# Kernel tuning notes

Hardware: AMD Instinct MI355X
Metric: run time of the kernel (lower is better)

Reference implementation:

```python
import jax, jax.numpy as jnp
from jax import lax
import numpy as np

IMG_W = 384; IMG_H = 384; FEAT = 24; RF = 16
RATIOS = (0.5, 1.0, 2.0); SCALES = (8.0, 16.0, 32.0)
K = 9                      # len(RATIOS) * len(SCALES)
N = FEAT * FEAT * K        # 5184 anchors/proposals
MID = 24; CIN = 512
NMS_THRESH = 0.7; MIN_SIZE = 16.0


def _make_anchors():
    # Faithful port of RPN._get_anchors (vectorized over the grid).
    area = float(RF * RF)
    base = []
    for r in RATIOS:
        cols = np.round(np.sqrt(area / r)); rows = np.round(cols * r)
        x0 = 0.5 * RF - 0.5 * (cols - 1); x1 = 0.5 * RF + 0.5 * (cols - 1)
        y0 = 0.5 * RF - 0.5 * (rows - 1); y1 = 0.5 * RF + 0.5 * (rows - 1)
        aw = x1 - x0 + 1; ah = y1 - y0 + 1
        acx = x0 + 0.5 * (aw - 1); acy = y0 + 0.5 * (ah - 1)
        for s in SCALES:
            nx0 = acx - 0.5 * (aw * s - 1.0); nx1 = acx + 0.5 * (aw * s - 1.0)
            ny0 = acy - 0.5 * (ah * s - 1.0); ny1 = acy + 0.5 * (ah * s - 1.0)
            w = nx1 - nx0 + 1; h = ny1 - ny0 + 1
            base.append([nx0 + 0.5 * (w - 1), ny0 + 0.5 * (h - 1), w, h])
    base = np.asarray(base, np.float32)  # (K,4) as (cx, cy, w, h)
    ii, jj = np.meshgrid(np.arange(FEAT), np.arange(FEAT), indexing='ij')
    g = np.broadcast_to(base, (FEAT, FEAT, K, 4)).copy()  # (H, W, K, 4)
    g[..., 0] += (jj * RF)[:, :, None]
    g[..., 1] += (ii * RF)[:, :, None]
    a = g.reshape(-1, 4)  # matches permute(1,2,0).reshape(-1,4) ordering
    ax0 = a[:, 0] - 0.5 * (a[:, 2] - 1.0); ay0 = a[:, 1] - 0.5 * (a[:, 3] - 1.0)
    ax1 = a[:, 2] + ax0 - 1.0; ay1 = a[:, 3] + ay0 - 1.0
    valid = (ax0 >= 0) & (ay0 >= 0) & (ax1 < IMG_W) & (ay1 < IMG_H)
    return jnp.asarray(a, jnp.float32), jnp.asarray(valid)


def setup_inputs() -> dict:
    key = jax.random.key(0)
    ks = jax.random.split(key, 6)
    anchors, valid_mask = _make_anchors()
    return {
        'x': jax.random.normal(ks[0], (1, CIN, FEAT, FEAT), jnp.float32),
        'labels_class': jax.random.randint(ks[1], (N,), 0, 21, jnp.int32),
        'W_rpn': jax.random.normal(ks[2], (MID, CIN, 3, 3), jnp.float32) * 0.02,
        'b_rpn': jnp.zeros((MID,), jnp.float32),
        'W_cls': jax.random.normal(ks[3], (2 * K, MID), jnp.float32) * 0.05,
        'b_cls': jnp.zeros((2 * K,), jnp.float32),
        'W_reg': jax.random.normal(ks[4], (4 * K, MID), jnp.float32) * 0.01,
        'b_reg': jnp.zeros((4 * K,), jnp.float32),
        'anchors': anchors,
        'valid_mask': valid_mask,
    }


def _forward(x, W_rpn, b_rpn, W_cls, b_cls, W_reg, b_reg, anchors, valid_mask, labels_class):
    # 3x3 conv + relu, then 1x1 cls/reg heads
    h = jax.nn.relu(
        lax.conv_general_dilated(x, W_rpn, (1, 1), ((1, 1), (1, 1)),
                                 dimension_numbers=('NCHW', 'OIHW', 'NCHW'))
        + b_rpn[None, :, None, None])
    cls_out = (jnp.einsum('nchw,oc->nohw', h, W_cls) + b_cls[None, :, None, None])[0]
    cls_out = cls_out.transpose(1, 2, 0).reshape(-1, 2)   # [N,2]
    reg_out = (jnp.einsum('nchw,oc->nohw', h, W_reg) + b_reg[None, :, None, None])[0]
    reg_out = reg_out.transpose(1, 2, 0).reshape(-1, 4)   # [N,4]

    # anchors -> proposals (cx, cy, w, h); computed for all anchors, validity masked below
    ax, ay, aw, ah = anchors[:, 0], anchors[:, 1], anchors[:, 2], anchors[:, 3]
    tx, ty, tw, th = reg_out[:, 0], reg_out[:, 1], reg_out[:, 2], reg_out[:, 3]
    px = ax + aw * tx; py = ay + ah * ty
    pw = aw * jnp.exp(tw); ph = ah * jnp.exp(th)
    proposals = jnp.stack((px, py, pw, ph), axis=1)

    # offset2bbox + clip_boxes
    x0 = px - 0.5 * (pw - 1.0); y0 = py - 0.5 * (ph - 1.0)
    x1 = pw + x0 - 1.0; y1 = ph + y0 - 1.0
    x0 = jnp.clip(x0, 0.0, IMG_W - 1.0); x1 = jnp.clip(x1, 0.0, IMG_W - 1.0)
    y0 = jnp.clip(y0, 0.0, IMG_H - 1.0); y1 = jnp.clip(y1, 0.0, IMG_H - 1.0)
    ws = x1 - x0 + 1.0; hs = y1 - y0 + 1.0

    probs = jax.nn.softmax(cls_out, axis=1)[:, 1]
    validity = valid_mask & (ws >= MIN_SIZE) & (hs >= MIN_SIZE)

    # greedy NMS (padded/masked: invalid boxes get score -1 and are never kept)
    scores = jnp.where(validity, probs, -1.0)
    order = jnp.argsort(-scores)
    bx0, by0, bx1, by1 = x0[order], y0[order], x1[order], y1[order]
    v_sorted = validity[order]
    areas = ws[order] * hs[order]
    iw = jnp.clip(jnp.minimum(bx1[:, None], bx1[None, :]) - jnp.maximum(bx0[:, None], bx0[None, :]) + 1.0, 0.0)
    ih = jnp.clip(jnp.minimum(by1[:, None], by1[None, :]) - jnp.maximum(by0[:, None], by0[None, :]) + 1.0, 0.0)
    inter = iw * ih
    iou = inter / (areas[:, None] + areas[None, :] - inter)  # [N,N]
    idxs = jnp.arange(N)

    def body(sup, xs):
        i, row, v = xs
        keep_i = v & jnp.logical_not(sup[i])
        sup = jnp.where(keep_i, sup | ((row > NMS_THRESH) & (idxs > i)), sup)
        return sup, keep_i

    _, keep_sorted = lax.scan(body, jnp.zeros((N,), bool), (idxs, iou, v_sorted))
    keep = jnp.zeros((N,), bool).at[order].set(keep_sorted)
    keepf = keep.astype(probs.dtype)

    # bbox2offset of kept boxes (padded: suppressed rows zeroed)
    filtered = jnp.stack((x0 + 0.5 * (ws - 1.0), y0 + 0.5 * (hs - 1.0), ws, hs), axis=1) * keepf[:, None]
    probs_kept = probs * keepf
    labels_kept = jnp.where(keep, labels_class, 0)
    return proposals, cls_out, filtered, probs_kept, labels_kept, keep


def reference(x, labels_class, W_rpn, b_rpn, W_cls, b_cls, W_reg, b_reg, anchors, valid_mask):
    return _forward(x, W_rpn, b_rpn, W_cls, b_cls, W_reg, b_reg, anchors, valid_mask, labels_class)
```

## Files before the change

kernel.cpp:

```cpp
#include <hip/hip_runtime.h>
#include <hip/hip_bf16.h>
#include <math.h>

#define NANC   5184
#define NPOS   576
#define CIN    512
#define MIDC   24
#define KANC   9
#define IMGW   384.0f
#define IMGM1  383.0f
#define MINSZ  16.0f
#define THRESH 0.7f

#define OFF_PROP 0
#define OFF_CLS  20736
#define OFF_FILT 31104
#define OFF_PK   51840
#define OFF_LBL  57024
#define OFF_KEEP 62208

#define MCAP 896
#define GCAP 14
#define TOTW (64 * (GCAP*(GCAP+1)/2))

#define WS_XT    0
#define WS_WT    1179648
#define WS_BOX   1622016
#define WS_PROB  1953792
#define WS_KEYS  2036736
#define WS_SIDX  2044928
#define WS_SBOX  2049024
#define WS_MASK  2063360
#define WS_CNT   2117120

__global__ __launch_bounds__(256) void k_prep(const float* __restrict__ x,
                                              const float* __restrict__ W,
                                              float* __restrict__ xt,
                                              float* __restrict__ Wt,
                                              unsigned* cnt) {
    int tid = blockIdx.x * 256 + threadIdx.x;
    if (tid == 0) *cnt = 0;
    const int TOT = CIN * NPOS + MIDC * CIN * 9;
    for (int idx = tid; idx < TOT; idx += gridDim.x * 256) {
        if (idx < CIN * NPOS) {
            int pos = idx >> 9, ic = idx & 511;
            xt[idx] = x[ic * NPOS + pos];
        } else {
            int k = idx - CIN * NPOS;
            int ic = k & 511; int t = k >> 9;
            int oc = t / 9, kk = t % 9;
            Wt[k] = W[(oc * CIN + ic) * 9 + kk];
        }
    }
}

__global__ __launch_bounds__(256) void k_main(
        const float* __restrict__ xt, const float* __restrict__ Wt,
        const float* __restrict__ brpn,
        const float* __restrict__ Wc, const float* __restrict__ bc,
        const float* __restrict__ Wr, const float* __restrict__ br,
        const float* __restrict__ anchors,
        float* __restrict__ out, float4* __restrict__ boxes,
        float* __restrict__ probs, unsigned long long* __restrict__ vkeys,
        unsigned* __restrict__ cnt) {
    const int tid = threadIdx.x;
    const int y = blockIdx.x / 6;
    const int xb = (blockIdx.x % 6) * 4;

    float acc[24][4];
    #pragma unroll
    for (int oc = 0; oc < 24; ++oc)
        #pragma unroll
        for (int p = 0; p < 4; ++p) acc[oc][p] = 0.f;

    for (int half = 0; half < 2; ++half) {
        const int ic = tid + half * 256;
        float xw[3][6];
        #pragma unroll
        for (int r = 0; r < 3; ++r) {
            int yy = y - 1 + r;
            #pragma unroll
            for (int c = 0; c < 6; ++c) {
                int xx = xb - 1 + c;
                bool in = (yy >= 0) & (yy < 24) & (xx >= 0) & (xx < 24);
                xw[r][c] = in ? xt[(yy * 24 + xx) * CIN + ic] : 0.f;
            }
        }
        const float* wp = Wt + ic;
        #pragma unroll
        for (int oc = 0; oc < 24; ++oc) {
            #pragma unroll
            for (int kk = 0; kk < 9; ++kk) {
                const int r = kk / 3, c = kk % 3;
                float wv = wp[(oc * 9 + kk) * CIN];
                #pragma unroll
                for (int p = 0; p < 4; ++p)
                    acc[oc][p] += wv * xw[r][c + p];
            }
        }
    }
    #pragma unroll
    for (int oc = 0; oc < 24; ++oc)
        #pragma unroll
        for (int p = 0; p < 4; ++p) {
            float v = acc[oc][p];
            #pragma unroll
            for (int m = 1; m < 64; m <<= 1) v += __shfl_xor(v, m, 64);
            acc[oc][p] = v;
        }

    __shared__ float red[4][96];
    __shared__ float h_ld[4 * 24];
    __shared__ float cls_ld[4 * 18];
    __shared__ float reg_ld[4 * 36];
    const int wave = tid >> 6, lane = tid & 63;
    if (lane == 0) {
        #pragma unroll
        for (int oc = 0; oc < 24; ++oc)
            #pragma unroll
            for (int p = 0; p < 4; ++p) red[wave][oc * 4 + p] = acc[oc][p];
    }
    __syncthreads();
    if (tid < 96) {
        float s = red[0][tid] + red[1][tid] + red[2][tid] + red[3][tid];
        int oc = tid >> 2, p = tid & 3;
        h_ld[p * 24 + oc] = fmaxf(s + brpn[oc], 0.f);
    }
    __syncthreads();
    if (tid < 216) {
        int p = tid / 54, o = tid % 54;
        const float* hv = h_ld + p * 24;
        if (o < 18) {
            float s = bc[o];
            const float* w = Wc + o * 24;
            #pragma unroll
            for (int c = 0; c < 24; ++c) s += w[c] * hv[c];
            cls_ld[p * 18 + o] = s;
            out[OFF_CLS + (y * 24 + xb + p) * 18 + o] = s;
        } else {
            int o2 = o - 18;
            float s = br[o2];
            const float* w = Wr + o2 * 24;
            #pragma unroll
            for (int c = 0; c < 24; ++c) s += w[c] * hv[c];
            reg_ld[p * 36 + o2] = s;
        }
    }
    __syncthreads();
    if (tid < 36) {
        #pragma clang fp contract(off)
        int p = tid / 9, k = tid % 9;
        int n = (y * 24 + xb + p) * 9 + k;
        float ax = anchors[4 * n], ay = anchors[4 * n + 1];
        float aw = anchors[4 * n + 2], ah = anchors[4 * n + 3];
        float tx = reg_ld[p * 36 + 4 * k],     ty = reg_ld[p * 36 + 4 * k + 1];
        float tw = reg_ld[p * 36 + 4 * k + 2], th = reg_ld[p * 36 + 4 * k + 3];
        float px = ax + aw * tx, py = ay + ah * ty;
        float pw = aw * expf(tw), ph = ah * expf(th);
        out[OFF_PROP + 4 * n]     = px;
        out[OFF_PROP + 4 * n + 1] = py;
        out[OFF_PROP + 4 * n + 2] = pw;
        out[OFF_PROP + 4 * n + 3] = ph;
        float gx0 = ax - 0.5f * (aw - 1.f);
        float gy0 = ay - 0.5f * (ah - 1.f);
        float gx1 = aw + gx0 - 1.f;
        float gy1 = ah + gy0 - 1.f;
        bool geo_ok = (gx0 >= 0.f) & (gy0 >= 0.f) & (gx1 < IMGW) & (gy1 < IMGW);
        float x0 = px - 0.5f * (pw - 1.f);
        float y0 = py - 0.5f * (ph - 1.f);
        float x1 = pw + x0 - 1.f;
        float y1 = ph + y0 - 1.f;
        x0 = fminf(fmaxf(x0, 0.f), IMGM1);
        x1 = fminf(fmaxf(x1, 0.f), IMGM1);
        y0 = fminf(fmaxf(y0, 0.f), IMGM1);
        y1 = fminf(fmaxf(y1, 0.f), IMGM1);
        float wsb = x1 - x0 + 1.f, hsb = y1 - y0 + 1.f;
        float c0 = cls_ld[p * 18 + 2 * k], c1 = cls_ld[p * 18 + 2 * k + 1];
        float mx = fmaxf(c0, c1);
        float e0 = expf(c0 - mx), e1 = expf(c1 - mx);
        float pr = e1 / (e0 + e1);
        boxes[n] = make_float4(x0, y0, x1, y1);
        probs[n] = pr;
        bool valid = geo_ok && (wsb >= MINSZ) && (hsb >= MINSZ);
        if (valid) {
            unsigned pos = atomicAdd(cnt, 1u);
            unsigned u = __float_as_uint(pr);
            unsigned enc = u ^ ((u >> 31) ? 0xFFFFFFFFu : 0x80000000u);
            vkeys[pos] = ((unsigned long long)(~enc) << 32) | (unsigned)n;
        }
    }
}

__global__ __launch_bounds__(64) void k_rank(const unsigned long long* __restrict__ vkeys,
                                             const unsigned* __restrict__ cnt,
                                             int* __restrict__ sidx,
                                             float4* __restrict__ sbox,
                                             const float4* __restrict__ boxes) {
    __shared__ unsigned long long keys[MCAP];
    const int t = threadIdx.x;
    unsigned Mc = *cnt; int M = (int)(Mc < (unsigned)MCAP ? Mc : (unsigned)MCAP);
    for (int i = t; i < M; i += 64) keys[i] = vkeys[i];
    __syncthreads();
    int i = blockIdx.x * 64 + t;
    if (i < M) {
        unsigned long long ki = keys[i];
        int r = 0;
        #pragma unroll 4
        for (int j = 0; j < M; ++j) r += (keys[j] < ki) ? 1 : 0;
        int n = (int)(ki & 0xFFFFFFFFu);
        sidx[r] = n;
        sbox[r] = boxes[n];
    }
}

__global__ __launch_bounds__(256) void k_mask(const float4* __restrict__ sbox,
                                              const unsigned* __restrict__ cnt,
                                              unsigned long long* __restrict__ mask) {
    __shared__ float4 sb[MCAP];
    const int t = threadIdx.x;
    for (int i = t; i < MCAP; i += 256) sb[i] = sbox[i];
    __syncthreads();
    unsigned Mc = *cnt; unsigned M = Mc < (unsigned)MCAP ? Mc : (unsigned)MCAP;
    int widx = blockIdx.x * 256 + t;
    if (widx >= TOTW) return;
    int g = 0, base = 0;
    while (g < GCAP - 1) {
        int nb = base + 64 * (GCAP - g);
        if (widx < nb) break;
        base = nb; ++g;
    }
    int rem = widx - base;
    int r = rem / (GCAP - g);
    int gw = g + rem % (GCAP - g);
    int i = g * 64 + r;
    if (i >= (int)M) return;
    {
        #pragma clang fp contract(off)
        float4 bi = sb[i];
        float ai = (bi.z - bi.x + 1.f) * (bi.w - bi.y + 1.f);
        unsigned long long w = 0;
        #pragma unroll 4
        for (int b = 0; b < 64; ++b) {
            int j = gw * 64 + b;
            if (j > i) {
                float4 bj = sb[j];
                float iw = fminf(bi.z, bj.z) - fmaxf(bi.x, bj.x) + 1.f;
                float ih = fminf(bi.w, bj.w) - fmaxf(bi.y, bj.y) + 1.f;
                iw = fmaxf(iw, 0.f); ih = fmaxf(ih, 0.f);
                float inter = iw * ih;
                float aj = (bj.z - bj.x + 1.f) * (bj.w - bj.y + 1.f);
                float iou = inter / (ai + aj - inter);
                if (iou > THRESH) w |= 1ULL << b;
            }
        }
        mask[widx] = w;
    }
}

__global__ __launch_bounds__(1024) void k_nms(const unsigned long long* __restrict__ mask_g,
                                              const int* __restrict__ sidx_g,
                                              const unsigned* __restrict__ cnt,
                                              const float4* __restrict__ boxes,
                                              const float* __restrict__ probs,
                                              const int* __restrict__ labels,
                                              float* __restrict__ out) {
    __shared__ unsigned long long mk[TOTW];
    __shared__ int sidx[MCAP];
    __shared__ unsigned long long keepm[81];
    __shared__ unsigned long long keeps[GCAP];
    __shared__ unsigned long long suppw[GCAP];
    const int t = threadIdx.x;
    unsigned Mc = *cnt; unsigned M = Mc < (unsigned)MCAP ? Mc : (unsigned)MCAP;
    for (int i = t; i < TOTW; i += 1024) mk[i] = mask_g[i];
    if (t < MCAP) sidx[t] = sidx_g[t];
    if (t < 81) keepm[t] = 0;
    if (t < GCAP) { keeps[t] = 0; suppw[t] = 0; }
    __syncthreads();
    const int wid = t >> 6, lane = t & 63;
    const int ngroups = (int)((M + 63) >> 6);
    for (int g = 0; g < ngroups; ++g) {
        const int rowstride = GCAP - g;
        const int base_g = 64 * (GCAP * g - (g * (g - 1)) / 2);
        int nbits = (int)M - g * 64; if (nbits > 64) nbits = 64;
        unsigned long long vmaskbits = (nbits < 64) ? ((1ULL << nbits) - 1ULL) : ~0ULL;
        if (wid == 0) {
            unsigned long long diag = mk[base_g + lane * rowstride];
            unsigned dlo = (unsigned)diag, dhi = (unsigned)(diag >> 32);
            unsigned long long supp = suppw[g];
            unsigned long long nz = __ballot(diag != 0ULL) & vmaskbits;
            while (nz) {
                int r = __ffsll(nz) - 1;
                nz &= nz - 1;
                if (!((supp >> r) & 1ULL)) {
                    unsigned rlo = (unsigned)__builtin_amdgcn_readlane((int)dlo, r);
                    unsigned rhi = (unsigned)__builtin_amdgcn_readlane((int)dhi, r);
                    supp |= ((unsigned long long)rhi << 32) | rlo;
                }
            }
            if (lane == 0) keeps[g] = ~supp & vmaskbits;
        }
        __syncthreads();
        if (wid > g && wid < GCAP) {
            unsigned long long kw = keeps[g];
            unsigned long long v = ((kw >> lane) & 1ULL)
                ? mk[base_g + lane * rowstride + (wid - g)] : 0ULL;
            unsigned vlo = (unsigned)v, vhi = (unsigned)(v >> 32);
            #pragma unroll
            for (int m = 1; m < 64; m <<= 1) {
                vlo |= __shfl_xor(vlo, m, 64);
                vhi |= __shfl_xor(vhi, m, 64);
            }
            if (lane == 0)
                suppw[wid] |= ((unsigned long long)vhi << 32) | vlo;
        }
        __syncthreads();
    }
    if (t < (int)M) {
        if ((keeps[t >> 6] >> (t & 63)) & 1ULL) {
            int n = sidx[t];
            atomicOr(&keepm[n >> 6], 1ULL << (n & 63));
        }
    }
    __syncthreads();
    for (int n = t; n < NANC; n += 1024) {
        unsigned long long kb = (keepm[n >> 6] >> (n & 63)) & 1ULL;
        float kf = kb ? 1.f : 0.f;
        float4 b = boxes[n];
        float wsb = b.z - b.x + 1.f, hsb = b.w - b.y + 1.f;
        float4 fo;
        fo.x = (b.x + 0.5f * (wsb - 1.f)) * kf;
        fo.y = (b.y + 0.5f * (hsb - 1.f)) * kf;
        fo.z = wsb * kf;
        fo.w = hsb * kf;
        *reinterpret_cast<float4*>(out + OFF_FILT + 4 * n) = fo;
        out[OFF_PK + n]  = probs[n] * kf;
        out[OFF_LBL + n] = kb ? (float)labels[n] : 0.f;
        out[OFF_KEEP + n] = kf;
    }
}

extern "C" void kernel_launch(void* const* d_in, const int* in_sizes, int n_in,
                              void* d_out, int out_size, void* d_ws, size_t ws_size,
                              hipStream_t stream) {
    const float* x        = (const float*)d_in[0];
    const int*   labels   = (const int*)d_in[1];
    const float* Wrpn     = (const float*)d_in[2];
    const float* brpn     = (const float*)d_in[3];
    const float* Wcls     = (const float*)d_in[4];
    const float* bcls     = (const float*)d_in[5];
    const float* Wreg     = (const float*)d_in[6];
    const float* breg     = (const float*)d_in[7];
    const float* anchors  = (const float*)d_in[8];
    float* out = (float*)d_out;
    char* ws = (char*)d_ws;

    float*  xt    = (float*)(ws + WS_XT);
    float*  Wt    = (float*)(ws + WS_WT);
    float4* boxes = (float4*)(ws + WS_BOX);
    float*  probs = (float*)(ws + WS_PROB);
    unsigned long long* vkeys = (unsigned long long*)(ws + WS_KEYS);
    int*    sidx  = (int*)(ws + WS_SIDX);
    float4* sbox  = (float4*)(ws + WS_SBOX);
    unsigned long long* mask = (unsigned long long*)(ws + WS_MASK);
    unsigned* cnt = (unsigned*)(ws + WS_CNT);

    k_prep<<<1584, 256, 0, stream>>>(x, Wrpn, xt, Wt, cnt);
    k_main<<<144, 256, 0, stream>>>(xt, Wt, brpn, Wcls, bcls, Wreg, breg,
                                    anchors, out, boxes, probs, vkeys, cnt);
    k_rank<<<GCAP, 64, 0, stream>>>(vkeys, cnt, sidx, sbox, boxes);
    k_mask<<<27, 256, 0, stream>>>(sbox, cnt, mask);
    k_nms<<<1, 1024, 0, stream>>>(mask, sidx, cnt, boxes, probs, labels, out);
}
```

Before: 149.6 us.

## Fuse five kernels into one persistent kernel with global atomic barriers

Replaces the prep, conv/head, rank, mask and NMS kernel launches with a single 144-block kernel that separates phases with software grid barriers built on atomic counters. A memset clears the counter, keep bitmap and barrier slots first. The aim is to remove per-launch overhead and the idle gaps between the small dependent kernels. In exchange, prep now uses only 144 blocks instead of 1584, the NMS phase runs on 256 threads instead of 1024, and the code relies on all 144 blocks being co-resident for the spin barriers to avoid deadlock.

```diff
diff --git a/kernel.cpp b/kernel.cpp
--- a/kernel.cpp
+++ b/kernel.cpp
@@ -6,7 +6,6 @@
 #define NPOS   576
 #define CIN    512
 #define MIDC   24
-#define KANC   9
 #define IMGW   384.0f
 #define IMGM1  383.0f
 #define MINSZ  16.0f
@@ -32,304 +31,321 @@
 #define WS_SBOX  2049024
 #define WS_MASK  2063360
 #define WS_CNT   2117120
-
-__global__ __launch_bounds__(256) void k_prep(const float* __restrict__ x,
-                                              const float* __restrict__ W,
-                                              float* __restrict__ xt,
-                                              float* __restrict__ Wt,
-                                              unsigned* cnt) {
-    int tid = blockIdx.x * 256 + threadIdx.x;
-    if (tid == 0) *cnt = 0;
-    const int TOT = CIN * NPOS + MIDC * CIN * 9;
-    for (int idx = tid; idx < TOT; idx += gridDim.x * 256) {
-        if (idx < CIN * NPOS) {
-            int pos = idx >> 9, ic = idx & 511;
-            xt[idx] = x[ic * NPOS + pos];
-        } else {
-            int k = idx - CIN * NPOS;
-            int ic = k & 511; int t = k >> 9;
-            int oc = t / 9, kk = t % 9;
-            Wt[k] = W[(oc * CIN + ic) * 9 + kk];
-        }
-    }
+#define WS_KEEPM 2117128
+#define WS_BAR   2117776
+#define ZERO_OFF WS_CNT
+#define ZERO_BYTES 688
+
+#define NB 144
+#define NT 256
+
+__device__ __forceinline__ void gbar(unsigned* bar, int s) {
+    __syncthreads();
+    if (threadIdx.x == 0) {
+        __threadfence();
+        atomicAdd(&bar[s], 1u);
+        while (atomicAdd(&bar[s], 0u) < (unsigned)NB)
+            __builtin_amdgcn_s_sleep(2);
+        __threadfence();
+    }
+    __syncthreads();
 }
 
-__global__ __launch_bounds__(256) void k_main(
-        const float* __restrict__ xt, const float* __restrict__ Wt,
+__global__ __launch_bounds__(NT) void k_all(
+        const float* __restrict__ x, const float* __restrict__ W,
         const float* __restrict__ brpn,
         const float* __restrict__ Wc, const float* __restrict__ bc,
         const float* __restrict__ Wr, const float* __restrict__ br,
-        const float* __restrict__ anchors,
-        float* __restrict__ out, float4* __restrict__ boxes,
-        float* __restrict__ probs, unsigned long long* __restrict__ vkeys,
-        unsigned* __restrict__ cnt) {
-    const int tid = threadIdx.x;
-    const int y = blockIdx.x / 6;
-    const int xb = (blockIdx.x % 6) * 4;
-
-    float acc[24][4];
-    #pragma unroll
-    for (int oc = 0; oc < 24; ++oc)
-        #pragma unroll
-        for (int p = 0; p < 4; ++p) acc[oc][p] = 0.f;
-
-    for (int half = 0; half < 2; ++half) {
-        const int ic = tid + half * 256;
-        float xw[3][6];
-        #pragma unroll
-        for (int r = 0; r < 3; ++r) {
-            int yy = y - 1 + r;
-            #pragma unroll
-            for (int c = 0; c < 6; ++c) {
-                int xx = xb - 1 + c;
-                bool in = (yy >= 0) & (yy < 24) & (xx >= 0) & (xx < 24);
-                xw[r][c] = in ? xt[(yy * 24 + xx) * CIN + ic] : 0.f;
-            }
-        }
-        const float* wp = Wt + ic;
-        #pragma unroll
-        for (int oc = 0; oc < 24; ++oc) {
-            #pragma unroll
-            for (int kk = 0; kk < 9; ++kk) {
-                const int r = kk / 3, c = kk % 3;
-                float wv = wp[(oc * 9 + kk) * CIN];
-                #pragma unroll
-                for (int p = 0; p < 4; ++p)
-                    acc[oc][p] += wv * xw[r][c + p];
-            }
-        }
-    }
-    #pragma unroll
-    for (int oc = 0; oc < 24; ++oc)
-        #pragma unroll
-        for (int p = 0; p < 4; ++p) {
-            float v = acc[oc][p];
-            #pragma unroll
-            for (int m = 1; m < 64; m <<= 1) v += __shfl_xor(v, m, 64);
-            acc[oc][p] = v;
-        }
+        const float* __restrict__ anchors, const int* __restrict__ labels,
+        float* __restrict__ out,
+        float* __restrict__ xt, float* __restrict__ Wt,
+        float4* __restrict__ boxes, float* __restrict__ probs,
+        unsigned long long* __restrict__ vkeys,
+        int* __restrict__ sidx_g, float4* __restrict__ sbox_g,
+        unsigned long long* __restrict__ mask_g,
+        unsigned* __restrict__ cnt, unsigned long long* __restrict__ keepm_g,
+        unsigned* __restrict__ bar) {
+    const int t = threadIdx.x;
+    const int b = blockIdx.x;
+    const int gtid = b * NT + t;
 
     __shared__ float red[4][96];
     __shared__ float h_ld[4 * 24];
     __shared__ float cls_ld[4 * 18];
     __shared__ float reg_ld[4 * 36];
-    const int wave = tid >> 6, lane = tid & 63;
-    if (lane == 0) {
+    __shared__ unsigned long long keys_s[MCAP];
+    __shared__ float4 sb_s[MCAP];
+    __shared__ unsigned long long mk_s[TOTW];
+    __shared__ unsigned long long keeps[GCAP];
+    __shared__ unsigned long long suppw[GCAP];
+
+    {
+        const int TOT = CIN * NPOS + MIDC * CIN * 9;
+        for (int idx = gtid; idx < TOT; idx += NB * NT) {
+            if (idx < CIN * NPOS) {
+                int pos = idx >> 9, ic = idx & 511;
+                xt[idx] = x[ic * NPOS + pos];
+            } else {
+                int k = idx - CIN * NPOS;
+                int ic = k & 511; int tt = k >> 9;
+                int oc = tt / 9, kk = tt % 9;
+                Wt[k] = W[(oc * CIN + ic) * 9 + kk];
+            }
+        }
+    }
+    gbar(bar, 0);
+
+    {
+        const int tid = t;
+        const int y = b / 6;
+        const int xb = (b % 6) * 4;
+
+        float acc[24][4];
         #pragma unroll
         for (int oc = 0; oc < 24; ++oc)
             #pragma unroll
-            for (int p = 0; p < 4; ++p) red[wave][oc * 4 + p] = acc[oc][p];
-    }
-    __syncthreads();
-    if (tid < 96) {
-        float s = red[0][tid] + red[1][tid] + red[2][tid] + red[3][tid];
-        int oc = tid >> 2, p = tid & 3;
-        h_ld[p * 24 + oc] = fmaxf(s + brpn[oc], 0.f);
-    }
-    __syncthreads();
-    if (tid < 216) {
-        int p = tid / 54, o = tid % 54;
-        const float* hv = h_ld + p * 24;
-        if (o < 18) {
-            float s = bc[o];
-            const float* w = Wc + o * 24;
-            #pragma unroll
-            for (int c = 0; c < 24; ++c) s += w[c] * hv[c];
-            cls_ld[p * 18 + o] = s;
-            out[OFF_CLS + (y * 24 + xb + p) * 18 + o] = s;
-        } else {
-            int o2 = o - 18;
-            float s = br[o2];
-            const float* w = Wr + o2 * 24;
-            #pragma unroll
-            for (int c = 0; c < 24; ++c) s += w[c] * hv[c];
-            reg_ld[p * 36 + o2] = s;
-        }
-    }
-    __syncthreads();
-    if (tid < 36) {
-        #pragma clang fp contract(off)
-        int p = tid / 9, k = tid % 9;
-        int n = (y * 24 + xb + p) * 9 + k;
-        float ax = anchors[4 * n], ay = anchors[4 * n + 1];
-        float aw = anchors[4 * n + 2], ah = anchors[4 * n + 3];
-        float tx = reg_ld[p * 36 + 4 * k],     ty = reg_ld[p * 36 + 4 * k + 1];
-        float tw = reg_ld[p * 36 + 4 * k + 2], th = reg_ld[p * 36 + 4 * k + 3];
-        float px = ax + aw * tx, py = ay + ah * ty;
-        float pw = aw * expf(tw), ph = ah * expf(th);
-        out[OFF_PROP + 4 * n]     = px;
-        out[OFF_PROP + 4 * n + 1] = py;
-        out[OFF_PROP + 4 * n + 2] = pw;
-        out[OFF_PROP + 4 * n + 3] = ph;
-        float gx0 = ax - 0.5f * (aw - 1.f);
-        float gy0 = ay - 0.5f * (ah - 1.f);
-        float gx1 = aw + gx0 - 1.f;
-        float gy1 = ah + gy0 - 1.f;
-        bool geo_ok = (gx0 >= 0.f) & (gy0 >= 0.f) & (gx1 < IMGW) & (gy1 < IMGW);
-        float x0 = px - 0.5f * (pw - 1.f);
-        float y0 = py - 0.5f * (ph - 1.f);
-        float x1 = pw + x0 - 1.f;
-        float y1 = ph + y0 - 1.f;
-        x0 = fminf(fmaxf(x0, 0.f), IMGM1);
-        x1 = fminf(fmaxf(x1, 0.f), IMGM1);
-        y0 = fminf(fmaxf(y0, 0.f), IMGM1);
-        y1 = fminf(fmaxf(y1, 0.f), IMGM1);
-        float wsb = x1 - x0 + 1.f, hsb = y1 - y0 + 1.f;
-        float c0 = cls_ld[p * 18 + 2 * k], c1 = cls_ld[p * 18 + 2 * k + 1];
-        float mx = fmaxf(c0, c1);
-        float e0 = expf(c0 - mx), e1 = expf(c1 - mx);
-        float pr = e1 / (e0 + e1);
-        boxes[n] = make_float4(x0, y0, x1, y1);
-        probs[n] = pr;
-        bool valid = geo_ok && (wsb >= MINSZ) && (hsb >= MINSZ);
-        if (valid) {
-            unsigned pos = atomicAdd(cnt, 1u);
-            unsigned u = __float_as_uint(pr);
-            unsigned enc = u ^ ((u >> 31) ? 0xFFFFFFFFu : 0x80000000u);
-            vkeys[pos] = ((unsigned long long)(~enc) << 32) | (unsigned)n;
-        }
-    }
-}
-
-__global__ __launch_bounds__(64) void k_rank(const unsigned long long* __restrict__ vkeys,
-                                             const unsigned* __restrict__ cnt,
-                                             int* __restrict__ sidx,
-                                             float4* __restrict__ sbox,
-                                             const float4* __restrict__ boxes) {
-    __shared__ unsigned long long keys[MCAP];
-    const int t = threadIdx.x;
-    unsigned Mc = *cnt; int M = (int)(Mc < (unsigned)MCAP ? Mc : (unsigned)MCAP);
-    for (int i = t; i < M; i += 64) keys[i] = vkeys[i];
-    __syncthreads();
-    int i = blockIdx.x * 64 + t;
-    if (i < M) {
-        unsigned long long ki = keys[i];
-        int r = 0;
-        #pragma unroll 4
-        for (int j = 0; j < M; ++j) r += (keys[j] < ki) ? 1 : 0;
-        int n = (int)(ki & 0xFFFFFFFFu);
-        sidx[r] = n;
-        sbox[r] = boxes[n];
-    }
-}
-
-__global__ __launch_bounds__(256) void k_mask(const float4* __restrict__ sbox,
-                                              const unsigned* __restrict__ cnt,
-                                              unsigned long long* __restrict__ mask) {
-    __shared__ float4 sb[MCAP];
-    const int t = threadIdx.x;
-    for (int i = t; i < MCAP; i += 256) sb[i] = sbox[i];
-    __syncthreads();
-    unsigned Mc = *cnt; unsigned M = Mc < (unsigned)MCAP ? Mc : (unsigned)MCAP;
-    int widx = blockIdx.x * 256 + t;
-    if (widx >= TOTW) return;
-    int g = 0, base = 0;
-    while (g < GCAP - 1) {
-        int nb = base + 64 * (GCAP - g);
-        if (widx < nb) break;
-        base = nb; ++g;
-    }
-    int rem = widx - base;
-    int r = rem / (GCAP - g);
-    int gw = g + rem % (GCAP - g);
-    int i = g * 64 + r;
-    if (i >= (int)M) return;
-    {
-        #pragma clang fp contract(off)
-        float4 bi = sb[i];
-        float ai = (bi.z - bi.x + 1.f) * (bi.w - bi.y + 1.f);
-        unsigned long long w = 0;
-        #pragma unroll 4
-        for (int b = 0; b < 64; ++b) {
-            int j = gw * 64 + b;
-            if (j > i) {
-                float4 bj = sb[j];
-                float iw = fminf(bi.z, bj.z) - fmaxf(bi.x, bj.x) + 1.f;
-                float ih = fminf(bi.w, bj.w) - fmaxf(bi.y, bj.y) + 1.f;
-                iw = fmaxf(iw, 0.f); ih = fmaxf(ih, 0.f);
-                float inter = iw * ih;
-                float aj = (bj.z - bj.x + 1.f) * (bj.w - bj.y + 1.f);
-                float iou = inter / (ai + aj - inter);
-                if (iou > THRESH) w |= 1ULL << b;
-            }
-        }
-        mask[widx] = w;
-    }
-}
-
-__global__ __launch_bounds__(1024) void k_nms(const unsigned long long* __restrict__ mask_g,
-                                              const int* __restrict__ sidx_g,
-                                              const unsigned* __restrict__ cnt,
-                                              const float4* __restrict__ boxes,
-                                              const float* __restrict__ probs,
-                                              const int* __restrict__ labels,
-                                              float* __restrict__ out) {
-    __shared__ unsigned long long mk[TOTW];
-    __shared__ int sidx[MCAP];
-    __shared__ unsigned long long keepm[81];
-    __shared__ unsigned long long keeps[GCAP];
-    __shared__ unsigned long long suppw[GCAP];
-    const int t = threadIdx.x;
-    unsigned Mc = *cnt; unsigned M = Mc < (unsigned)MCAP ? Mc : (unsigned)MCAP;
-    for (int i = t; i < TOTW; i += 1024) mk[i] = mask_g[i];
-    if (t < MCAP) sidx[t] = sidx_g[t];
-    if (t < 81) keepm[t] = 0;
-    if (t < GCAP) { keeps[t] = 0; suppw[t] = 0; }
-    __syncthreads();
-    const int wid = t >> 6, lane = t & 63;
-    const int ngroups = (int)((M + 63) >> 6);
-    for (int g = 0; g < ngroups; ++g) {
-        const int rowstride = GCAP - g;
-        const int base_g = 64 * (GCAP * g - (g * (g - 1)) / 2);
-        int nbits = (int)M - g * 64; if (nbits > 64) nbits = 64;
-        unsigned long long vmaskbits = (nbits < 64) ? ((1ULL << nbits) - 1ULL) : ~0ULL;
-        if (wid == 0) {
-            unsigned long long diag = mk[base_g + lane * rowstride];
-            unsigned dlo = (unsigned)diag, dhi = (unsigned)(diag >> 32);
-            unsigned long long supp = suppw[g];
-            unsigned long long nz = __ballot(diag != 0ULL) & vmaskbits;
-            while (nz) {
-                int r = __ffsll(nz) - 1;
-                nz &= nz - 1;
-                if (!((supp >> r) & 1ULL)) {
-                    unsigned rlo = (unsigned)__builtin_amdgcn_readlane((int)dlo, r);
-                    unsigned rhi = (unsigned)__builtin_amdgcn_readlane((int)dhi, r);
-                    supp |= ((unsigned long long)rhi << 32) | rlo;
-                }
-            }
-            if (lane == 0) keeps[g] = ~supp & vmaskbits;
-        }
-        __syncthreads();
-        if (wid > g && wid < GCAP) {
-            unsigned long long kw = keeps[g];
-            unsigned long long v = ((kw >> lane) & 1ULL)
-                ? mk[base_g + lane * rowstride + (wid - g)] : 0ULL;
-            unsigned vlo = (unsigned)v, vhi = (unsigned)(v >> 32);
-            #pragma unroll
-            for (int m = 1; m < 64; m <<= 1) {
-                vlo |= __shfl_xor(vlo, m, 64);
-                vhi |= __shfl_xor(vhi, m, 64);
-            }
-            if (lane == 0)
-                suppw[wid] |= ((unsigned long long)vhi << 32) | vlo;
-        }
-        __syncthreads();
-    }
-    if (t < (int)M) {
-        if ((keeps[t >> 6] >> (t & 63)) & 1ULL) {
-            int n = sidx[t];
-            atomicOr(&keepm[n >> 6], 1ULL << (n & 63));
-        }
-    }
-    __syncthreads();
-    for (int n = t; n < NANC; n += 1024) {
-        unsigned long long kb = (keepm[n >> 6] >> (n & 63)) & 1ULL;
+            for (int p = 0; p < 4; ++p) acc[oc][p] = 0.f;
+
+        for (int half = 0; half < 2; ++half) {
+            const int ic = tid + half * 256;
+            float xw[3][6];
+            #pragma unroll
+            for (int r = 0; r < 3; ++r) {
+                int yy = y - 1 + r;
+                #pragma unroll
+                for (int c = 0; c < 6; ++c) {
+                    int xx = xb - 1 + c;
+                    bool in = (yy >= 0) & (yy < 24) & (xx >= 0) & (xx < 24);
+                    xw[r][c] = in ? xt[(yy * 24 + xx) * CIN + ic] : 0.f;
+                }
+            }
+            const float* wp = Wt + ic;
+            #pragma unroll
+            for (int oc = 0; oc < 24; ++oc) {
+                #pragma unroll
+                for (int kk = 0; kk < 9; ++kk) {
+                    const int r = kk / 3, c = kk % 3;
+                    float wv = wp[(oc * 9 + kk) * CIN];
+                    #pragma unroll
+                    for (int p = 0; p < 4; ++p)
+                        acc[oc][p] += wv * xw[r][c + p];
+                }
+            }
+        }
+        #pragma unroll
+        for (int oc = 0; oc < 24; ++oc)
+            #pragma unroll
+            for (int p = 0; p < 4; ++p) {
+                float v = acc[oc][p];
+                #pragma unroll
+                for (int m = 1; m < 64; m <<= 1) v += __shfl_xor(v, m, 64);
+                acc[oc][p] = v;
+            }
+
+        const int wave = tid >> 6, lane = tid & 63;
+        if (lane == 0) {
+            #pragma unroll
+            for (int oc = 0; oc < 24; ++oc)
+                #pragma unroll
+                for (int p = 0; p < 4; ++p) red[wave][oc * 4 + p] = acc[oc][p];
+        }
+        __syncthreads();
+        if (tid < 96) {
+            float s = red[0][tid] + red[1][tid] + red[2][tid] + red[3][tid];
+            int oc = tid >> 2, p = tid & 3;
+            h_ld[p * 24 + oc] = fmaxf(s + brpn[oc], 0.f);
+        }
+        __syncthreads();
+        if (tid < 216) {
+            int p = tid / 54, o = tid % 54;
+            const float* hv = h_ld + p * 24;
+            if (o < 18) {
+                float s = bc[o];
+                const float* w = Wc + o * 24;
+                #pragma unroll
+                for (int c = 0; c < 24; ++c) s += w[c] * hv[c];
+                cls_ld[p * 18 + o] = s;
+                out[OFF_CLS + (y * 24 + xb + p) * 18 + o] = s;
+            } else {
+                int o2 = o - 18;
+                float s = br[o2];
+                const float* w = Wr + o2 * 24;
+                #pragma unroll
+                for (int c = 0; c < 24; ++c) s += w[c] * hv[c];
+                reg_ld[p * 36 + o2] = s;
+            }
+        }
+        __syncthreads();
+        if (tid < 36) {
+            #pragma clang fp contract(off)
+            int p = tid / 9, k = tid % 9;
+            int n = (y * 24 + xb + p) * 9 + k;
+            float ax = anchors[4 * n], ay = anchors[4 * n + 1];
+            float aw = anchors[4 * n + 2], ah = anchors[4 * n + 3];
+            float tx = reg_ld[p * 36 + 4 * k],     ty = reg_ld[p * 36 + 4 * k + 1];
+            float tw = reg_ld[p * 36 + 4 * k + 2], th = reg_ld[p * 36 + 4 * k + 3];
+            float px = ax + aw * tx, py = ay + ah * ty;
+            float pw = aw * expf(tw), ph = ah * expf(th);
+            out[OFF_PROP + 4 * n]     = px;
+            out[OFF_PROP + 4 * n + 1] = py;
+            out[OFF_PROP + 4 * n + 2] = pw;
+            out[OFF_PROP + 4 * n + 3] = ph;
+            float gx0 = ax - 0.5f * (aw - 1.f);
+            float gy0 = ay - 0.5f * (ah - 1.f);
+            float gx1 = aw + gx0 - 1.f;
+            float gy1 = ah + gy0 - 1.f;
+            bool geo_ok = (gx0 >= 0.f) & (gy0 >= 0.f) & (gx1 < IMGW) & (gy1 < IMGW);
+            float x0 = px - 0.5f * (pw - 1.f);
+            float y0 = py - 0.5f * (ph - 1.f);
+            float x1 = pw + x0 - 1.f;
+            float y1 = ph + y0 - 1.f;
+            x0 = fminf(fmaxf(x0, 0.f), IMGM1);
+            x1 = fminf(fmaxf(x1, 0.f), IMGM1);
+            y0 = fminf(fmaxf(y0, 0.f), IMGM1);
+            y1 = fminf(fmaxf(y1, 0.f), IMGM1);
+            float wsb = x1 - x0 + 1.f, hsb = y1 - y0 + 1.f;
+            float c0 = cls_ld[p * 18 + 2 * k], c1 = cls_ld[p * 18 + 2 * k + 1];
+            float mx = fmaxf(c0, c1);
+            float e0 = expf(c0 - mx), e1 = expf(c1 - mx);
+            float pr = e1 / (e0 + e1);
+            boxes[n] = make_float4(x0, y0, x1, y1);
+            probs[n] = pr;
+            bool valid = geo_ok && (wsb >= MINSZ) && (hsb >= MINSZ);
+            if (valid) {
+                unsigned pos = atomicAdd(cnt, 1u);
+                unsigned u = __float_as_uint(pr);
+                unsigned enc = u ^ ((u >> 31) ? 0xFFFFFFFFu : 0x80000000u);
+                vkeys[pos] = ((unsigned long long)(~enc) << 32) | (unsigned)n;
+            }
+        }
+    }
+    gbar(bar, 1);
+
+    unsigned Mc = *cnt;
+    int M = (int)(Mc < (unsigned)MCAP ? Mc : (unsigned)MCAP);
+
+    if (b < GCAP) {
+        for (int i = t; i < MCAP; i += NT)
+            keys_s[i] = (i < M) ? vkeys[i] : ~0ULL;
+        __syncthreads();
+        if (t < 64) {
+            int i = b * 64 + t;
+            if (i < M) {
+                unsigned long long ki = keys_s[i];
+                int r = 0;
+                #pragma unroll 4
+                for (int j = 0; j < M; ++j) r += (keys_s[j] < ki) ? 1 : 0;
+                int n = (int)(ki & 0xFFFFFFFFu);
+                sidx_g[r] = n;
+                sbox_g[r] = boxes[n];
+            }
+        }
+    }
+    gbar(bar, 2);
+
+    if (b * NT < TOTW) {
+        for (int i = t; i < MCAP; i += NT)
+            sb_s[i] = (i < M) ? sbox_g[i] : make_float4(0.f, 0.f, 0.f, 0.f);
+        __syncthreads();
+        int widx = b * NT + t;
+        if (widx < TOTW) {
+            int g = 0, base = 0;
+            while (g < GCAP - 1) {
+                int nb2 = base + 64 * (GCAP - g);
+                if (widx < nb2) break;
+                base = nb2; ++g;
+            }
+            int rem = widx - base;
+            int r = rem / (GCAP - g);
+            int gw = g + rem % (GCAP - g);
+            int i = g * 64 + r;
+            if (i >= M) {
+                mask_g[widx] = 0ULL;
+            } else {
+                #pragma clang fp contract(off)
+                float4 bi = sb_s[i];
+                float ai = (bi.z - bi.x + 1.f) * (bi.w - bi.y + 1.f);
+                unsigned long long w = 0;
+                #pragma unroll 4
+                for (int bb = 0; bb < 64; ++bb) {
+                    int j = gw * 64 + bb;
+                    if (j > i) {
+                        float4 bj = sb_s[j];
+                        float iw = fminf(bi.z, bj.z) - fmaxf(bi.x, bj.x) + 1.f;
+                        float ih = fminf(bi.w, bj.w) - fmaxf(bi.y, bj.y) + 1.f;
+                        iw = fmaxf(iw, 0.f); ih = fmaxf(ih, 0.f);
+                        float inter = iw * ih;
+                        float aj = (bj.z - bj.x + 1.f) * (bj.w - bj.y + 1.f);
+                        float iou = inter / (ai + aj - inter);
+                        if (iou > THRESH) w |= 1ULL << bb;
+                    }
+                }
+                mask_g[widx] = w;
+            }
+        }
+    }
+    gbar(bar, 3);
+
+    if (b == 0) {
+        for (int i = t; i < TOTW; i += NT) mk_s[i] = mask_g[i];
+        if (t < GCAP) { keeps[t] = 0; suppw[t] = 0; }
+        __syncthreads();
+        const int wid = t >> 6, lane = t & 63;
+        const int ngroups = (M + 63) >> 6;
+        for (int g = 0; g < ngroups; ++g) {
+            const int rowstride = GCAP - g;
+            const int base_g = 64 * (GCAP * g - (g * (g - 1)) / 2);
+            int nbits = M - g * 64; if (nbits > 64) nbits = 64;
+            unsigned long long vmaskbits = (nbits < 64) ? ((1ULL << nbits) - 1ULL) : ~0ULL;
+            if (wid == 0) {
+                unsigned long long diag = mk_s[base_g + lane * rowstride];
+                unsigned dlo = (unsigned)diag, dhi = (unsigned)(diag >> 32);
+                unsigned long long supp = suppw[g];
+                unsigned long long nz = __ballot(diag != 0ULL) & vmaskbits;
+                while (nz) {
+                    int r = __ffsll(nz) - 1;
+                    nz &= nz - 1;
+                    if (!((supp >> r) & 1ULL)) {
+                        unsigned rlo = (unsigned)__builtin_amdgcn_readlane((int)dlo, r);
+                        unsigned rhi = (unsigned)__builtin_amdgcn_readlane((int)dhi, r);
+                        supp |= ((unsigned long long)rhi << 32) | rlo;
+                    }
+                }
+                if (lane == 0) keeps[g] = ~supp & vmaskbits;
+            }
+            __syncthreads();
+            for (int h = g + 1 + wid; h < GCAP; h += 4) {
+                unsigned long long kw = keeps[g];
+                unsigned long long v = ((kw >> lane) & 1ULL)
+                    ? mk_s[base_g + lane * rowstride + (h - g)] : 0ULL;
+                unsigned vlo = (unsigned)v, vhi = (unsigned)(v >> 32);
+                #pragma unroll
+                for (int m = 1; m < 64; m <<= 1) {
+                    vlo |= __shfl_xor(vlo, m, 64);
+                    vhi |= __shfl_xor(vhi, m, 64);
+                }
+                if (lane == 0)
+                    suppw[h] |= ((unsigned long long)vhi << 32) | vlo;
+            }
+            __syncthreads();
+        }
+        for (int i = t; i < M; i += NT) {
+            if ((keeps[i >> 6] >> (i & 63)) & 1ULL) {
+                int n = sidx_g[i];
+                atomicOr(&keepm_g[n >> 6], 1ULL << (n & 63));
+            }
+        }
+    }
+    gbar(bar, 4);
+
+    for (int n = gtid; n < NANC; n += NB * NT) {
+        unsigned long long kb = (keepm_g[n >> 6] >> (n & 63)) & 1ULL;
         float kf = kb ? 1.f : 0.f;
-        float4 b = boxes[n];
-        float wsb = b.z - b.x + 1.f, hsb = b.w - b.y + 1.f;
+        float4 bx = boxes[n];
+        float wsb = bx.z - bx.x + 1.f, hsb = bx.w - bx.y + 1.f;
         float4 fo;
-        fo.x = (b.x + 0.5f * (wsb - 1.f)) * kf;
-        fo.y = (b.y + 0.5f * (hsb - 1.f)) * kf;
+        fo.x = (bx.x + 0.5f * (wsb - 1.f)) * kf;
+        fo.y = (bx.y + 0.5f * (hsb - 1.f)) * kf;
         fo.z = wsb * kf;
         fo.w = hsb * kf;
         *reinterpret_cast<float4*>(out + OFF_FILT + 4 * n) = fo;
@@ -363,11 +379,12 @@
     float4* sbox  = (float4*)(ws + WS_SBOX);
     unsigned long long* mask = (unsigned long long*)(ws + WS_MASK);
     unsigned* cnt = (unsigned*)(ws + WS_CNT);
-
-    k_prep<<<1584, 256, 0, stream>>>(x, Wrpn, xt, Wt, cnt);
-    k_main<<<144, 256, 0, stream>>>(xt, Wt, brpn, Wcls, bcls, Wreg, breg,
-                                    anchors, out, boxes, probs, vkeys, cnt);
-    k_rank<<<GCAP, 64, 0, stream>>>(vkeys, cnt, sidx, sbox, boxes);
-    k_mask<<<27, 256, 0, stream>>>(sbox, cnt, mask);
-    k_nms<<<1, 1024, 0, stream>>>(mask, sidx, cnt, boxes, probs, labels, out);
+    unsigned long long* keepm = (unsigned long long*)(ws + WS_KEEPM);
+    unsigned* bar = (unsigned*)(ws + WS_BAR);
+
+    hipMemsetAsync(ws + ZERO_OFF, 0, ZERO_BYTES, stream);
+    k_all<<<NB, NT, 0, stream>>>(x, Wrpn, brpn, Wcls, bcls, Wreg, breg,
+                                 anchors, labels, out,
+                                 xt, Wt, boxes, probs, vkeys, sidx, sbox,
+                                 mask, cnt, keepm, bar);
 }
```

After: 184.4 us. 1.23x slower.
